# Performance work log

Hardware: AMD Instinct MI355X
Metric: run time of the kernel (lower is better)

The kernel has to match this reference:

```python
import jax, jax.numpy as jnp
import numpy as np

B, T, N, K1, H, C = 2, 8, 5000, 17, 4, 16  # K1 = self + 16 neighbors
N_OUT = (C + 1) // 2


def setup_inputs() -> dict:
    key = jax.random.key(0)
    kf, kn, km = jax.random.split(key, 3)
    # small scale so exp(-||Mdf||^2) stays in a numerically interesting range
    features = jax.random.normal(kf, (B, T, N, H, C), dtype=jnp.float32) * 0.1
    nearest = jax.random.randint(kn, (N, K1), 0, N, dtype=jnp.int32)
    nearest = nearest.at[:, 0].set(jnp.arange(N, dtype=jnp.int32))  # col 0 = self
    drop = (jax.random.uniform(km, (N, K1)) < 0.05) & (jnp.arange(K1)[None, :] > 0)
    nearest = jnp.where(drop, jnp.int32(-1), nearest)
    # faithful parameter init: [I | 0] blocks scaled by Q1_init / Q2_init, diag(M_init)
    q_form = jnp.zeros((H, N_OUT, C), dtype=jnp.float32).at[:, :, :N_OUT].set(jnp.eye(N_OUT, dtype=jnp.float32))
    multiQ1 = q_form * 1.2
    multiQ2 = q_form * 0.8
    multiM = jnp.broadcast_to(jnp.eye(C, dtype=jnp.float32), (H, C, C)) * 1.5
    return {"features": features, "nearest_nodes": nearest,
            "multiQ1": multiQ1, "multiQ2": multiQ2, "multiM": multiM}


def reference(features, nearest_nodes, multiQ1, multiQ2, multiM):
    B_, T_, N_, H_, C_ = features.shape
    # pad row N_ is all-zeros; -1 sentinel indices are routed to it
    pad = jnp.concatenate([features, jnp.zeros_like(features[:, :, :1])], axis=2)  # (B,T,N+1,H,C)
    idx = jnp.where(nearest_nodes < 0, N_, nearest_nodes)  # (N, K1)

    # ---------------- undirected ----------------
    nbr = idx[:, 1:]                       # (N, K) neighbor indices (excl. self)
    fj = pad[:, :, nbr]                    # (B,T,N,K,H,C) gathered neighbor feats
    df = features[:, :, :, None] - fj      # (B,T,N,K,H,C)
    Mdf = jnp.einsum('hij,btnkhj->btnkhi', multiM, df)
    w = jnp.exp(-jnp.sum(Mdf * Mdf, axis=-1))              # (B,T,N,K,H)
    valid = (nearest_nodes[:, 1:] >= 0)[None, None, :, :, None]
    w = w * valid
    deg = jnp.sum(w, axis=3)                               # (B,T,N,H)
    pad_deg = jnp.concatenate([deg, jnp.zeros_like(deg[:, :, :1])], axis=2)
    deg_j = pad_deg[:, :, nbr]                             # (B,T,N,K,H)
    dmul = jnp.sqrt(deg[:, :, :, None] * deg_j)
    inv = jnp.where(dmul > 0, 1.0 / jnp.where(dmul > 0, dmul, 1.0), 0.0)
    u_w = w * inv                                          # (B,T,N,K,H)

    # ---------------- directed ----------------
    fi = pad[:, :-1, idx]                                  # (B,T-1,N,K1,H,C)
    Qi = jnp.einsum('hij,btnkhj->btnkhi', multiQ1, fi)     # (B,T-1,N,K1,H,n_out)
    Qj = jnp.einsum('hij,btnhj->btnhi', multiQ2, features[:, 1:])  # (B,T-1,N,H,n_out)
    wd = jnp.exp(-jnp.sum(Qi * Qj[:, :, :, None], axis=-1))        # (B,T-1,N,K1,H)
    wd = wd * (nearest_nodes >= 0)[None, None, :, :, None]
    in_deg = jnp.sum(wd, axis=3)                           # (B,T-1,N,H)
    inv_d = jnp.where(in_deg > 0, 1.0 / jnp.where(in_deg > 0, in_deg, 1.0), 0.0)
    d_w = wd * inv_d[:, :, :, None]                        # (B,T-1,N,K1,H)

    return (u_w, d_w)
```

## Files before the change

### kernel.cpp

```cpp
#include <hip/hip_runtime.h>
#include <cstdio>

#define BB 2
#define TT 8
#define NNODE 5000
#define KK1 17
#define HH 4
#define NT (BB*TT*NNODE)
#define NREST (BB*7*NNODE)

typedef unsigned short u16;
typedef unsigned int u32;

__device__ __forceinline__ u16 f2bf(float x) {
  u32 u = __float_as_uint(x);
  u32 r = (u + 0x7fffu + ((u >> 16) & 1u)) >> 16;
  return (u16)r;
}
__device__ __forceinline__ float bfLo(u32 w){ return __uint_as_float(w << 16); }
__device__ __forceinline__ float bfHi(u32 w){ return __uint_as_float(w & 0xffff0000u); }

__device__ __forceinline__ float edge_e(uint4 A0, uint4 A1, uint4 B0, uint4 B1) {
  u32 aw[8] = {A0.x,A0.y,A0.z,A0.w,A1.x,A1.y,A1.z,A1.w};
  u32 bw[8] = {B0.x,B0.y,B0.z,B0.w,B1.x,B1.y,B1.z,B1.w};
  float dot = 0.f, si = 0.f, sj = 0.f;
#pragma unroll
  for (int r = 0; r < 8; ++r) {
    float al = bfLo(aw[r]), ah = bfHi(aw[r]);
    float bl = bfLo(bw[r]), bh = bfHi(bw[r]);
    dot = fmaf(al, bl, dot); dot = fmaf(ah, bh, dot);
    si  = fmaf(al, al, si);  si  = fmaf(ah, ah, si);
    sj  = fmaf(bl, bl, sj);  sj  = fmaf(bh, bh, sj);
  }
  return si + sj - 2.f*dot;
}

__global__ void __launch_bounds__(256) k_prep(
    const float* __restrict__ feat, const float* __restrict__ mm,
    const float* __restrict__ q1, const float* __restrict__ q2,
    u16* __restrict__ g, u16* __restrict__ a8, u16* __restrict__ b8) {
  const int lane = threadIdx.x & 63;
  const int h = lane >> 4, i = lane & 15;
  const int bid = blockIdx.x;
  const int x = bid & 7;
  const int local = (bid >> 3) * 4 + (threadIdx.x >> 6);
  const int mbase = x * 10000 + local * 10;
  float Mrow[16], Qrow[16];
  const float* qsrc = (i < 8) ? (q1 + (h*8 + i)*16) : (q2 + (h*8 + (i - 8))*16);
#pragma unroll
  for (int j = 0; j < 16; ++j) {
    Mrow[j] = mm[(h*16 + i)*16 + j];
    Qrow[j] = qsrc[j];
  }
  for (int l = 0; l < 10; ++l) {
    const int m = mbase + l;
    const float4* fp = reinterpret_cast<const float4*>(feat + (size_t)m*64 + h*16);
    float fv[16];
#pragma unroll
    for (int q = 0; q < 4; ++q) {
      float4 v = fp[q];
      fv[q*4+0] = v.x; fv[q*4+1] = v.y; fv[q*4+2] = v.z; fv[q*4+3] = v.w;
    }
    float accG = 0.f, accQ = 0.f;
#pragma unroll
    for (int j = 0; j < 16; ++j) {
      accG = fmaf(Mrow[j], fv[j], accG);
      accQ = fmaf(Qrow[j], fv[j], accQ);
    }
    g[(size_t)m*64 + lane] = f2bf(accG);
    if (i < 8) a8[(size_t)m*32 + h*8 + i] = f2bf(accQ);
    else       b8[(size_t)m*32 + h*8 + (i - 8)] = f2bf(accQ);
  }
}

__global__ void __launch_bounds__(256) k_deg(
    const u16* __restrict__ g, const int* __restrict__ nn,
    float* __restrict__ deg, u16* __restrict__ wbuf) {
  const int bid = blockIdx.x;
  const int work = ((bid & 7) * 1250) + (bid >> 3);
  const int p = work*4 + (threadIdx.x >> 6);
  const int m0 = p*2, m1 = m0 + 1;
  const int lane = threadIdx.x & 63;
  const int k = lane >> 2, h = lane & 3;
  const int n0 = m0 % NNODE, n1 = m1 % NNODE;
  const int bt0 = m0 - n0, bt1 = m1 - n1;
  int jr0 = nn[n0*KK1 + 1 + k];
  int jr1 = nn[n1*KK1 + 1 + k];
  bool v0 = jr0 >= 0, v1 = jr1 >= 0;
  int j0 = v0 ? jr0 : 0;
  int j1 = v1 ? jr1 : 0;
  const uint4* pi0 = reinterpret_cast<const uint4*>(g + (size_t)m0*64 + h*16);
  const uint4* pi1 = reinterpret_cast<const uint4*>(g + (size_t)m1*64 + h*16);
  const uint4* pj0 = reinterpret_cast<const uint4*>(g + (size_t)(bt0 + j0)*64 + h*16);
  const uint4* pj1 = reinterpret_cast<const uint4*>(g + (size_t)(bt1 + j1)*64 + h*16);
  uint4 A00 = pi0[0], A01 = pi0[1];
  uint4 A10 = pi1[0], A11 = pi1[1];
  uint4 B00 = pj0[0], B01 = pj0[1];
  uint4 B10 = pj1[0], B11 = pj1[1];
  float e0 = edge_e(A00, A01, B00, B01);
  float e1 = edge_e(A10, A11, B10, B11);
  float w0 = v0 ? __expf(-e0) : 0.f;
  float w1 = v1 ? __expf(-e1) : 0.f;
  wbuf[(size_t)m0*64 + lane] = f2bf(w0);
  wbuf[(size_t)m1*64 + lane] = f2bf(w1);
  float d0 = w0, d1 = w1;
  d0 += __shfl_xor(d0, 4);  d1 += __shfl_xor(d1, 4);
  d0 += __shfl_xor(d0, 8);  d1 += __shfl_xor(d1, 8);
  d0 += __shfl_xor(d0, 16); d1 += __shfl_xor(d1, 16);
  d0 += __shfl_xor(d0, 32); d1 += __shfl_xor(d1, 32);
  if (lane < 4) {
    deg[m0*4 + lane] = d0;
    deg[m1*4 + lane] = d1;
  }
}

__global__ void __launch_bounds__(256) k_uw(
    const u16* __restrict__ wbuf, const int* __restrict__ nn,
    const float* __restrict__ deg, float* __restrict__ uw) {
  const int bid = blockIdx.x;
  const int x = bid & 7, sub = bid >> 3;
  const int wg = (x < 4 ? x*313 : 4*313 + (x-4)*312) + sub;
  const int idx8 = (wg * 256 + threadIdx.x) * 8;
  const int m = idx8 >> 6;
  const int r8 = idx8 & 63;
  const int k0 = r8 >> 2;
  const int n = m % NNODE;
  const int btb = m - n;
  uint4 wv = *reinterpret_cast<const uint4*>(wbuf + idx8);
  int jr0 = nn[n*KK1 + 1 + k0];
  int jr1 = nn[n*KK1 + 2 + k0];
  float4 di = *reinterpret_cast<const float4*>(deg + (size_t)m*4);
  float4 o0 = {0.f,0.f,0.f,0.f}, o1 = {0.f,0.f,0.f,0.f};
  if (jr0 >= 0) {
    float4 dj = *reinterpret_cast<const float4*>(deg + (size_t)(btb + jr0)*4);
    float w0 = bfLo(wv.x), w1 = bfHi(wv.x), w2 = bfLo(wv.y), w3 = bfHi(wv.y);
    float p0 = di.x*dj.x, p1 = di.y*dj.y, p2 = di.z*dj.z, p3 = di.w*dj.w;
    o0.x = (w0 > 0.f && p0 > 0.f) ? w0 * rsqrtf(p0) : 0.f;
    o0.y = (w1 > 0.f && p1 > 0.f) ? w1 * rsqrtf(p1) : 0.f;
    o0.z = (w2 > 0.f && p2 > 0.f) ? w2 * rsqrtf(p2) : 0.f;
    o0.w = (w3 > 0.f && p3 > 0.f) ? w3 * rsqrtf(p3) : 0.f;
  }
  if (jr1 >= 0) {
    float4 dj = *reinterpret_cast<const float4*>(deg + (size_t)(btb + jr1)*4);
    float w0 = bfLo(wv.z), w1 = bfHi(wv.z), w2 = bfLo(wv.w), w3 = bfHi(wv.w);
    float p0 = di.x*dj.x, p1 = di.y*dj.y, p2 = di.z*dj.z, p3 = di.w*dj.w;
    o1.x = (w0 > 0.f && p0 > 0.f) ? w0 * rsqrtf(p0) : 0.f;
    o1.y = (w1 > 0.f && p1 > 0.f) ? w1 * rsqrtf(p1) : 0.f;
    o1.z = (w2 > 0.f && p2 > 0.f) ? w2 * rsqrtf(p2) : 0.f;
    o1.w = (w3 > 0.f && p3 > 0.f) ? w3 * rsqrtf(p3) : 0.f;
  }
  *reinterpret_cast<float4*>(uw + idx8)     = o0;
  *reinterpret_cast<float4*>(uw + idx8 + 4) = o1;
}

__global__ void __launch_bounds__(256) k_dw(
    const u16* __restrict__ a8, const u16* __restrict__ b8,
    const int* __restrict__ nn, float* __restrict__ dw) {
  __shared__ float lds[64*68];
  const int bid = blockIdx.x;
  const int x = bid & 7, sub = bid >> 3;
  const int wg = (x < 6 ? x*137 : 6*137 + (x-6)*136) + sub;
  const int lr = threadIdx.x >> 2;
  const int h  = threadIdx.x & 3;
  const int rest = wg*64 + lr;
  if (rest < NREST) {
    const int n = rest % NNODE;
    const int q2 = rest / NNODE;
    const int b = q2 / 7, t = q2 % 7;
    uint4 Bv = *reinterpret_cast<const uint4*>(b8 + ((size_t)((b*TT + t + 1)*NNODE + n))*32 + h*8);
    float bv[8] = {bfLo(Bv.x), bfHi(Bv.x), bfLo(Bv.y), bfHi(Bv.y),
                   bfLo(Bv.z), bfHi(Bv.z), bfLo(Bv.w), bfHi(Bv.w)};
    const int nbase = n*KK1;
    const int abase = (b*TT + t)*NNODE;
    float wk[17];
    float indeg = 0.f;
#pragma unroll
    for (int kk = 0; kk < KK1; ++kk) {
      int jr = nn[nbase + kk];
      bool valid = jr >= 0;
      int j = valid ? jr : 0;
      uint4 Av = *reinterpret_cast<const uint4*>(a8 + ((size_t)(abase + j))*32 + h*8);
      float dot = 0.f;
      dot = fmaf(bfLo(Av.x), bv[0], dot); dot = fmaf(bfHi(Av.x), bv[1], dot);
      dot = fmaf(bfLo(Av.y), bv[2], dot); dot = fmaf(bfHi(Av.y), bv[3], dot);
      dot = fmaf(bfLo(Av.z), bv[4], dot); dot = fmaf(bfHi(Av.z), bv[5], dot);
      dot = fmaf(bfLo(Av.w), bv[6], dot); dot = fmaf(bfHi(Av.w), bv[7], dot);
      float w = valid ? __expf(-dot) : 0.f;
      wk[kk] = w;
      indeg += w;
    }
    float inv = (indeg > 0.f) ? (1.0f / indeg) : 0.f;
#pragma unroll
    for (int kk = 0; kk < KK1; ++kk) lds[lr*68 + kk*4 + h] = wk[kk] * inv;
  }
  __syncthreads();
  const int rows = NREST - wg*64;
  const int nchunks = (rows >= 64 ? 64 : rows) * 17;
  float4* obase = reinterpret_cast<float4*>(dw + (size_t)wg*4352);
  for (int c = threadIdx.x; c < nchunks; c += 256) {
    const int row = c / 17;
    const int col = (c % 17) * 4;
    obase[c] = *reinterpret_cast<const float4*>(&lds[row*68 + col]);
  }
}

extern "C" void kernel_launch(void* const* d_in, const int* in_sizes, int n_in,
                              void* d_out, int out_size, void* d_ws, size_t ws_size,
                              hipStream_t stream) {
  const float* feat = (const float*)d_in[0];
  const int*   nn   = (const int*)d_in[1];
  const float* q1   = (const float*)d_in[2];
  const float* q2   = (const float*)d_in[3];
  const float* mm   = (const float*)d_in[4];
  float* uw = (float*)d_out;
  float* dw = uw + (size_t)NT*64;
  u16*   wstage = (u16*)dw;

  const size_t G_BYTES  = (size_t)NT*64*2;
  const size_t A_BYTES  = (size_t)NT*32*2;
  const size_t DEG_BYTES= (size_t)NT*4*4;
  const size_t NEED = G_BYTES + 2*A_BYTES + DEG_BYTES;
  if (ws_size < NEED) {
    fprintf(stderr, "kernel_launch: ws_size %zu < needed %zu\n", ws_size, NEED);
    return;
  }
  u16*   g   = (u16*)d_ws;
  u16*   a8  = (u16*)((char*)d_ws + G_BYTES);
  u16*   b8  = (u16*)((char*)d_ws + G_BYTES + A_BYTES);
  float* deg = (float*)((char*)d_ws + G_BYTES + 2*A_BYTES);

  k_prep<<<2000, 256, 0, stream>>>(feat, mm, q1, q2, g, a8, b8);
  k_deg <<<10000, 256, 0, stream>>>(g, nn, deg, wstage);
  k_uw  <<<2500, 256, 0, stream>>>(wstage, nn, deg, uw);
  k_dw  <<<1094, 256, 0, stream>>>(a8, b8, nn, dw);
}
```

Baseline: 61.29 us.

## Fuse directed-weight kernel into degree kernel and stage weights in-place in uw

Merges the directed-weight computation into the degree kernel as extra blocks of one launch, removing a launch and letting both workloads overlap on the GPU. The bf16 undirected weights are now staged inside the uw output region at a layout that k_uw reads back and overwrites in place, so the dw region no longer serves as scratch. Degree blocks now handle the same node across two adjacent (b,t) slices, sharing one neighbor-index load, and the dw path loads neighbor indices once per quad and distributes them with shuffles. The in-place staging relies on each k_uw thread reading its staged slot before writing the same region, and the mixed-role kernel carries the LDS allocation into the degree blocks too.

```diff
diff --git a/kernel.cpp b/kernel.cpp
--- a/kernel.cpp
+++ b/kernel.cpp
@@ -8,6 +8,8 @@
 #define HH 4
 #define NT (BB*TT*NNODE)
 #define NREST (BB*7*NNODE)
+#define DEG_BLOCKS 10000
+#define DW_BLOCKS 1094
 
 typedef unsigned short u16;
 typedef unsigned int u32;
@@ -52,6 +54,7 @@
     Mrow[j] = mm[(h*16 + i)*16 + j];
     Qrow[j] = qsrc[j];
   }
+#pragma unroll 2
   for (int l = 0; l < 10; ++l) {
     const int m = mbase + l;
     const float4* fp = reinterpret_cast<const float4*>(feat + (size_t)m*64 + h*16);
@@ -73,50 +76,117 @@
   }
 }
 
-__global__ void __launch_bounds__(256) k_deg(
-    const u16* __restrict__ g, const int* __restrict__ nn,
-    float* __restrict__ deg, u16* __restrict__ wbuf) {
+__global__ void __launch_bounds__(256) k_degdw(
+    const u16* __restrict__ g, const u16* __restrict__ a8, const u16* __restrict__ b8,
+    const int* __restrict__ nn, float* __restrict__ deg,
+    u16* __restrict__ wstage, float* __restrict__ dw) {
+  __shared__ float lds[64*68];
   const int bid = blockIdx.x;
-  const int work = ((bid & 7) * 1250) + (bid >> 3);
-  const int p = work*4 + (threadIdx.x >> 6);
-  const int m0 = p*2, m1 = m0 + 1;
-  const int lane = threadIdx.x & 63;
-  const int k = lane >> 2, h = lane & 3;
-  const int n0 = m0 % NNODE, n1 = m1 % NNODE;
-  const int bt0 = m0 - n0, bt1 = m1 - n1;
-  int jr0 = nn[n0*KK1 + 1 + k];
-  int jr1 = nn[n1*KK1 + 1 + k];
-  bool v0 = jr0 >= 0, v1 = jr1 >= 0;
-  int j0 = v0 ? jr0 : 0;
-  int j1 = v1 ? jr1 : 0;
-  const uint4* pi0 = reinterpret_cast<const uint4*>(g + (size_t)m0*64 + h*16);
-  const uint4* pi1 = reinterpret_cast<const uint4*>(g + (size_t)m1*64 + h*16);
-  const uint4* pj0 = reinterpret_cast<const uint4*>(g + (size_t)(bt0 + j0)*64 + h*16);
-  const uint4* pj1 = reinterpret_cast<const uint4*>(g + (size_t)(bt1 + j1)*64 + h*16);
-  uint4 A00 = pi0[0], A01 = pi0[1];
-  uint4 A10 = pi1[0], A11 = pi1[1];
-  uint4 B00 = pj0[0], B01 = pj0[1];
-  uint4 B10 = pj1[0], B11 = pj1[1];
-  float e0 = edge_e(A00, A01, B00, B01);
-  float e1 = edge_e(A10, A11, B10, B11);
-  float w0 = v0 ? __expf(-e0) : 0.f;
-  float w1 = v1 ? __expf(-e1) : 0.f;
-  wbuf[(size_t)m0*64 + lane] = f2bf(w0);
-  wbuf[(size_t)m1*64 + lane] = f2bf(w1);
-  float d0 = w0, d1 = w1;
-  d0 += __shfl_xor(d0, 4);  d1 += __shfl_xor(d1, 4);
-  d0 += __shfl_xor(d0, 8);  d1 += __shfl_xor(d1, 8);
-  d0 += __shfl_xor(d0, 16); d1 += __shfl_xor(d1, 16);
-  d0 += __shfl_xor(d0, 32); d1 += __shfl_xor(d1, 32);
-  if (lane < 4) {
-    deg[m0*4 + lane] = d0;
-    deg[m1*4 + lane] = d1;
+  if (bid < DEG_BLOCKS) {
+    const int x = bid & 7;
+    const int n = (bid >> 3)*4 + (threadIdx.x >> 6);
+    const int lane = threadIdx.x & 63;
+    const int k = lane >> 2, h = lane & 3;
+    const int m0 = (2*x)*NNODE + n;
+    const int m1 = m0 + NNODE;
+    int jr = nn[n*KK1 + 1 + k];
+    bool v = jr >= 0;
+    int j = v ? jr : 0;
+    const uint4* pi0 = reinterpret_cast<const uint4*>(g + (size_t)m0*64 + h*16);
+    const uint4* pi1 = reinterpret_cast<const uint4*>(g + (size_t)m1*64 + h*16);
+    const uint4* pj0 = reinterpret_cast<const uint4*>(g + (size_t)((2*x)*NNODE + j)*64 + h*16);
+    const uint4* pj1 = reinterpret_cast<const uint4*>(g + (size_t)((2*x+1)*NNODE + j)*64 + h*16);
+    uint4 A00 = pi0[0], A01 = pi0[1];
+    uint4 A10 = pi1[0], A11 = pi1[1];
+    uint4 B00 = pj0[0], B01 = pj0[1];
+    uint4 B10 = pj1[0], B11 = pj1[1];
+    float e0 = edge_e(A00, A01, B00, B01);
+    float e1 = edge_e(A10, A11, B10, B11);
+    float w0 = v ? __expf(-e0) : 0.f;
+    float w1 = v ? __expf(-e1) : 0.f;
+    const int soff = ((lane >> 3) << 4) + (lane & 7);
+    wstage[(size_t)m0*128 + soff] = f2bf(w0);
+    wstage[(size_t)m1*128 + soff] = f2bf(w1);
+    float d0 = w0, d1 = w1;
+    d0 += __shfl_xor(d0, 4);  d1 += __shfl_xor(d1, 4);
+    d0 += __shfl_xor(d0, 8);  d1 += __shfl_xor(d1, 8);
+    d0 += __shfl_xor(d0, 16); d1 += __shfl_xor(d1, 16);
+    d0 += __shfl_xor(d0, 32); d1 += __shfl_xor(d1, 32);
+    if (lane < 4) {
+      deg[m0*4 + lane] = d0;
+      deg[m1*4 + lane] = d1;
+    }
+  } else {
+    const int wg = bid - DEG_BLOCKS;
+    const int lr = threadIdx.x >> 2;
+    const int h  = threadIdx.x & 3;
+    const int lane = threadIdx.x & 63;
+    const int qbase = lane & ~3;
+    const int rest = wg*64 + lr;
+    if (rest < NREST) {
+      const int n = rest % NNODE;
+      const int q2 = rest / NNODE;
+      const int b = q2 / 7, t = q2 % 7;
+      uint4 Bv = *reinterpret_cast<const uint4*>(b8 + ((size_t)((b*TT + t + 1)*NNODE + n))*32 + h*8);
+      float bv[8] = {bfLo(Bv.x), bfHi(Bv.x), bfLo(Bv.y), bfHi(Bv.y),
+                     bfLo(Bv.z), bfHi(Bv.z), bfLo(Bv.w), bfHi(Bv.w)};
+      const int nbase = n*KK1;
+      const int abase = (b*TT + t)*NNODE;
+      int jvec[4];
+      jvec[0] = nn[nbase + h + 0];
+      jvec[1] = nn[nbase + h + 4];
+      jvec[2] = nn[nbase + h + 8];
+      jvec[3] = nn[nbase + h + 12];
+      int j16 = nn[nbase + 16];
+      float wk[17];
+      float indeg = 0.f;
+#pragma unroll
+      for (int kk = 0; kk < 16; ++kk) {
+        int jr = __shfl(jvec[kk >> 2], qbase + (kk & 3));
+        bool valid = jr >= 0;
+        int j = valid ? jr : 0;
+        uint4 Av = *reinterpret_cast<const uint4*>(a8 + ((size_t)(abase + j))*32 + h*8);
+        float dot = 0.f;
+        dot = fmaf(bfLo(Av.x), bv[0], dot); dot = fmaf(bfHi(Av.x), bv[1], dot);
+        dot = fmaf(bfLo(Av.y), bv[2], dot); dot = fmaf(bfHi(Av.y), bv[3], dot);
+        dot = fmaf(bfLo(Av.z), bv[4], dot); dot = fmaf(bfHi(Av.z), bv[5], dot);
+        dot = fmaf(bfLo(Av.w), bv[6], dot); dot = fmaf(bfHi(Av.w), bv[7], dot);
+        float w = valid ? __expf(-dot) : 0.f;
+        wk[kk] = w;
+        indeg += w;
+      }
+      {
+        bool valid = j16 >= 0;
+        int j = valid ? j16 : 0;
+        uint4 Av = *reinterpret_cast<const uint4*>(a8 + ((size_t)(abase + j))*32 + h*8);
+        float dot = 0.f;
+        dot = fmaf(bfLo(Av.x), bv[0], dot); dot = fmaf(bfHi(Av.x), bv[1], dot);
+        dot = fmaf(bfLo(Av.y), bv[2], dot); dot = fmaf(bfHi(Av.y), bv[3], dot);
+        dot = fmaf(bfLo(Av.z), bv[4], dot); dot = fmaf(bfHi(Av.z), bv[5], dot);
+        dot = fmaf(bfLo(Av.w), bv[6], dot); dot = fmaf(bfHi(Av.w), bv[7], dot);
+        float w = valid ? __expf(-dot) : 0.f;
+        wk[16] = w;
+        indeg += w;
+      }
+      float inv = (indeg > 0.f) ? (1.0f / indeg) : 0.f;
+#pragma unroll
+      for (int kk = 0; kk < KK1; ++kk) lds[lr*68 + kk*4 + h] = wk[kk] * inv;
+    }
+    __syncthreads();
+    const int rows = NREST - wg*64;
+    const int nchunks = (rows >= 64 ? 64 : rows) * 17;
+    float4* obase = reinterpret_cast<float4*>(dw + (size_t)wg*4352);
+    for (int c = threadIdx.x; c < nchunks; c += 256) {
+      const int row = c / 17;
+      const int col = (c % 17) * 4;
+      obase[c] = *reinterpret_cast<const float4*>(&lds[row*68 + col]);
+    }
   }
 }
 
 __global__ void __launch_bounds__(256) k_uw(
-    const u16* __restrict__ wbuf, const int* __restrict__ nn,
-    const float* __restrict__ deg, float* __restrict__ uw) {
+    const int* __restrict__ nn, const float* __restrict__ deg,
+    float* __restrict__ uw) {
   const int bid = blockIdx.x;
   const int x = bid & 7, sub = bid >> 3;
   const int wg = (x < 4 ? x*313 : 4*313 + (x-4)*312) + sub;
@@ -126,82 +196,32 @@
   const int k0 = r8 >> 2;
   const int n = m % NNODE;
   const int btb = m - n;
-  uint4 wv = *reinterpret_cast<const uint4*>(wbuf + idx8);
+  uint4 wv = *reinterpret_cast<const uint4*>(uw + idx8);
   int jr0 = nn[n*KK1 + 1 + k0];
   int jr1 = nn[n*KK1 + 2 + k0];
   float4 di = *reinterpret_cast<const float4*>(deg + (size_t)m*4);
-  float4 o0 = {0.f,0.f,0.f,0.f}, o1 = {0.f,0.f,0.f,0.f};
+  uint4 o0 = {0u,0u,0u,0u}, o1 = {0u,0u,0u,0u};
   if (jr0 >= 0) {
     float4 dj = *reinterpret_cast<const float4*>(deg + (size_t)(btb + jr0)*4);
     float w0 = bfLo(wv.x), w1 = bfHi(wv.x), w2 = bfLo(wv.y), w3 = bfHi(wv.y);
     float p0 = di.x*dj.x, p1 = di.y*dj.y, p2 = di.z*dj.z, p3 = di.w*dj.w;
-    o0.x = (w0 > 0.f && p0 > 0.f) ? w0 * rsqrtf(p0) : 0.f;
-    o0.y = (w1 > 0.f && p1 > 0.f) ? w1 * rsqrtf(p1) : 0.f;
-    o0.z = (w2 > 0.f && p2 > 0.f) ? w2 * rsqrtf(p2) : 0.f;
-    o0.w = (w3 > 0.f && p3 > 0.f) ? w3 * rsqrtf(p3) : 0.f;
+    o0.x = __float_as_uint((w0 > 0.f && p0 > 0.f) ? w0 * rsqrtf(p0) : 0.f);
+    o0.y = __float_as_uint((w1 > 0.f && p1 > 0.f) ? w1 * rsqrtf(p1) : 0.f);
+    o0.z = __float_as_uint((w2 > 0.f && p2 > 0.f) ? w2 * rsqrtf(p2) : 0.f);
+    o0.w = __float_as_uint((w3 > 0.f && p3 > 0.f) ? w3 * rsqrtf(p3) : 0.f);
   }
   if (jr1 >= 0) {
     float4 dj = *reinterpret_cast<const float4*>(deg + (size_t)(btb + jr1)*4);
     float w0 = bfLo(wv.z), w1 = bfHi(wv.z), w2 = bfLo(wv.w), w3 = bfHi(wv.w);
     float p0 = di.x*dj.x, p1 = di.y*dj.y, p2 = di.z*dj.z, p3 = di.w*dj.w;
-    o1.x = (w0 > 0.f && p0 > 0.f) ? w0 * rsqrtf(p0) : 0.f;
-    o1.y = (w1 > 0.f && p1 > 0.f) ? w1 * rsqrtf(p1) : 0.f;
-    o1.z = (w2 > 0.f && p2 > 0.f) ? w2 * rsqrtf(p2) : 0.f;
-    o1.w = (w3 > 0.f && p3 > 0.f) ? w3 * rsqrtf(p3) : 0.f;
-  }
-  *reinterpret_cast<float4*>(uw + idx8)     = o0;
-  *reinterpret_cast<float4*>(uw + idx8 + 4) = o1;
-}
-
-__global__ void __launch_bounds__(256) k_dw(
-    const u16* __restrict__ a8, const u16* __restrict__ b8,
-    const int* __restrict__ nn, float* __restrict__ dw) {
-  __shared__ float lds[64*68];
-  const int bid = blockIdx.x;
-  const int x = bid & 7, sub = bid >> 3;
-  const int wg = (x < 6 ? x*137 : 6*137 + (x-6)*136) + sub;
-  const int lr = threadIdx.x >> 2;
-  const int h  = threadIdx.x & 3;
-  const int rest = wg*64 + lr;
-  if (rest < NREST) {
-    const int n = rest % NNODE;
-    const int q2 = rest / NNODE;
-    const int b = q2 / 7, t = q2 % 7;
-    uint4 Bv = *reinterpret_cast<const uint4*>(b8 + ((size_t)((b*TT + t + 1)*NNODE + n))*32 + h*8);
-    float bv[8] = {bfLo(Bv.x), bfHi(Bv.x), bfLo(Bv.y), bfHi(Bv.y),
-                   bfLo(Bv.z), bfHi(Bv.z), bfLo(Bv.w), bfHi(Bv.w)};
-    const int nbase = n*KK1;
-    const int abase = (b*TT + t)*NNODE;
-    float wk[17];
-    float indeg = 0.f;
-#pragma unroll
-    for (int kk = 0; kk < KK1; ++kk) {
-      int jr = nn[nbase + kk];
-      bool valid = jr >= 0;
-      int j = valid ? jr : 0;
-      uint4 Av = *reinterpret_cast<const uint4*>(a8 + ((size_t)(abase + j))*32 + h*8);
-      float dot = 0.f;
-      dot = fmaf(bfLo(Av.x), bv[0], dot); dot = fmaf(bfHi(Av.x), bv[1], dot);
-      dot = fmaf(bfLo(Av.y), bv[2], dot); dot = fmaf(bfHi(Av.y), bv[3], dot);
-      dot = fmaf(bfLo(Av.z), bv[4], dot); dot = fmaf(bfHi(Av.z), bv[5], dot);
-      dot = fmaf(bfLo(Av.w), bv[6], dot); dot = fmaf(bfHi(Av.w), bv[7], dot);
-      float w = valid ? __expf(-dot) : 0.f;
-      wk[kk] = w;
-      indeg += w;
-    }
-    float inv = (indeg > 0.f) ? (1.0f / indeg) : 0.f;
-#pragma unroll
-    for (int kk = 0; kk < KK1; ++kk) lds[lr*68 + kk*4 + h] = wk[kk] * inv;
-  }
-  __syncthreads();
-  const int rows = NREST - wg*64;
-  const int nchunks = (rows >= 64 ? 64 : rows) * 17;
-  float4* obase = reinterpret_cast<float4*>(dw + (size_t)wg*4352);
-  for (int c = threadIdx.x; c < nchunks; c += 256) {
-    const int row = c / 17;
-    const int col = (c % 17) * 4;
-    obase[c] = *reinterpret_cast<const float4*>(&lds[row*68 + col]);
-  }
+    o1.x = __float_as_uint((w0 > 0.f && p0 > 0.f) ? w0 * rsqrtf(p0) : 0.f);
+    o1.y = __float_as_uint((w1 > 0.f && p1 > 0.f) ? w1 * rsqrtf(p1) : 0.f);
+    o1.z = __float_as_uint((w2 > 0.f && p2 > 0.f) ? w2 * rsqrtf(p2) : 0.f);
+    o1.w = __float_as_uint((w3 > 0.f && p3 > 0.f) ? w3 * rsqrtf(p3) : 0.f);
+  }
+  uint4* ob = reinterpret_cast<uint4*>(uw + idx8);
+  ob[0] = o0;
+  ob[1] = o1;
 }
 
 extern "C" void kernel_launch(void* const* d_in, const int* in_sizes, int n_in,
@@ -214,7 +234,6 @@
   const float* mm   = (const float*)d_in[4];
   float* uw = (float*)d_out;
   float* dw = uw + (size_t)NT*64;
-  u16*   wstage = (u16*)dw;
 
   const size_t G_BYTES  = (size_t)NT*64*2;
   const size_t A_BYTES  = (size_t)NT*32*2;
@@ -228,9 +247,9 @@
   u16*   a8  = (u16*)((char*)d_ws + G_BYTES);
   u16*   b8  = (u16*)((char*)d_ws + G_BYTES + A_BYTES);
   float* deg = (float*)((char*)d_ws + G_BYTES + 2*A_BYTES);
-
-  k_prep<<<2000, 256, 0, stream>>>(feat, mm, q1, q2, g, a8, b8);
-  k_deg <<<10000, 256, 0, stream>>>(g, nn, deg, wstage);
-  k_uw  <<<2500, 256, 0, stream>>>(wstage, nn, deg, uw);
-  k_dw  <<<1094, 256, 0, stream>>>(a8, b8, nn, dw);
-}
+  u16*   wstage = (u16*)uw;
+
+  k_prep <<<2000, 256, 0, stream>>>(feat, mm, q1, q2, g, a8, b8);
+  k_degdw<<<DEG_BLOCKS + DW_BLOCKS, 256, 0, stream>>>(g, a8, b8, nn, deg, wstage, dw);
+  k_uw   <<<2500, 256, 0, stream>>>(nn, deg, uw);
+}
```

New measurement: 62.19 us. No clear change (+1.5%).
